# Kernel optimization log

Measured on AMD Instinct MI355X. Metric: run time of the kernel, lower is better.

Reference implementation:

```python
import jax, jax.numpy as jnp
import numpy as np

WH, WW = 12, 12
N_TOK = WH * WW          # 144
DIM = 512
HEADS = 16
NW = 64                  # windows per image
B_ = 256                 # num_windows * batch
CPB_HIDDEN = 512


def _rel_tables():
    # continuous relative coords table (SwinV2 cpb input), shape (1, 2Wh-1, 2Ww-1, 2)
    ch = np.arange(-(WH - 1), WH, dtype=np.float32)
    cw = np.arange(-(WW - 1), WW, dtype=np.float32)
    gh, gw = np.meshgrid(ch, cw, indexing='ij')
    table = np.stack([gh, gw], axis=-1)[None]
    table[..., 0] /= (WH - 1)
    table[..., 1] /= (WW - 1)
    table *= 8.0
    table = np.sign(table) * np.log2(np.abs(table) + 1.0) / np.log2(8.0)
    # relative position index, shape (N, N), values in [0, (2Wh-1)*(2Ww-1))
    coords = np.stack(np.meshgrid(np.arange(WH), np.arange(WW), indexing='ij'))
    cf = coords.reshape(2, -1)
    rel = (cf[:, :, None] - cf[:, None, :]).transpose(1, 2, 0).astype(np.int64)
    rel[..., 0] += WH - 1
    rel[..., 1] += WW - 1
    rel[..., 0] *= 2 * WW - 1
    idx = rel.sum(-1)
    return table.astype(np.float32), idx


def setup_inputs() -> dict:
    key = jax.random.key(0)
    ks = jax.random.split(key, 10)
    table, idx = _rel_tables()
    x = jax.random.normal(ks[0], (B_, N_TOK, DIM), dtype=jnp.float32)
    # 0 / -100 additive mask (shifted-window style), shape (nW, N, N)
    mask = jnp.where(jax.random.uniform(ks[1], (NW, N_TOK, N_TOK)) < 0.9, 0.0, -100.0).astype(jnp.float32)
    s = 0.02
    return {
        'x': x,
        'mask': mask,
        'qkv_w': s * jax.random.normal(ks[2], (3 * DIM, DIM), dtype=jnp.float32),
        'qkv_b': jnp.zeros((3 * DIM,), dtype=jnp.float32),
        'proj_w': s * jax.random.normal(ks[3], (DIM, DIM), dtype=jnp.float32),
        'proj_b': jnp.zeros((DIM,), dtype=jnp.float32),
        'cpb_w1': s * jax.random.normal(ks[4], (CPB_HIDDEN, 2), dtype=jnp.float32),
        'cpb_b1': jnp.zeros((CPB_HIDDEN,), dtype=jnp.float32),
        'cpb_w2': s * jax.random.normal(ks[5], (HEADS, CPB_HIDDEN), dtype=jnp.float32),
        'rel_table': jnp.asarray(table),
        'rel_index': jnp.asarray(idx, dtype=jnp.int32),
    }


def reference(x, mask, qkv_w, qkv_b, proj_w, proj_b, cpb_w1, cpb_b1, cpb_w2, rel_table, rel_index):
    Bw, N, C = x.shape
    H = cpb_w2.shape[0]
    hd = C // H
    scale = hd ** -0.5
    qkv = (x @ qkv_w.T + qkv_b).reshape(Bw, N, 3, H, hd).transpose(2, 0, 3, 1, 4)
    q, k, v = qkv[0], qkv[1], qkv[2]          # each (Bw, H, N, hd)
    attn = jnp.einsum('bhnd,bhmd->bhnm', q * scale, k)
    # continuous relative position bias: MLP on coord table then gather
    tbl = jax.nn.relu(rel_table @ cpb_w1.T + cpb_b1) @ cpb_w2.T   # (1, 2Wh-1, 2Ww-1, H)
    tbl = tbl.reshape(-1, H)
    bias = tbl[rel_index.reshape(-1)].reshape(N, N, H).transpose(2, 0, 1)  # (H, N, N)
    attn = attn + bias[None]
    nW = mask.shape[0]
    attn = attn.reshape(Bw // nW, nW, H, N, N) + mask[None, :, None]
    attn = jax.nn.softmax(attn.reshape(Bw, H, N, N), axis=-1)
    out = jnp.einsum('bhnm,bhmd->bhnd', attn, v).transpose(0, 2, 1, 3).reshape(Bw, N, C)
    return out @ proj_w.T + proj_b
```

## Files before the change

### kernel.cpp

```cpp
#include <hip/hip_runtime.h>


using f32x4  = __attribute__((ext_vector_type(4))) float;
using bf16x8 = __attribute__((ext_vector_type(8))) short;

__device__ __forceinline__ unsigned short f2bf(float f) {
  unsigned u = __float_as_uint(f);
  u = (u + 0x7fffu + ((u >> 16) & 1u)) >> 16;
  return (unsigned short)u;
}
__device__ __forceinline__ float bf2f(unsigned short s) {
  return __uint_as_float(((unsigned)s) << 16);
}

typedef __attribute__((address_space(1))) unsigned int as1_u32;
typedef __attribute__((address_space(3))) unsigned int as3_u32;

__device__ __forceinline__ void gll16(const void* g, void* l) {
  __builtin_amdgcn_global_load_lds((const as1_u32*)g, (as3_u32*)l, 16, 0, 0);
}

__global__ void cvt_f32_bf16(const float4* __restrict__ in,
                             unsigned short* __restrict__ out, int n4) {
  int i = blockIdx.x * blockDim.x + threadIdx.x;
  int stride = gridDim.x * blockDim.x;
  for (; i < n4; i += stride) {
    float4 v = in[i];
    ushort4 o;
    o.x = f2bf(v.x); o.y = f2bf(v.y); o.z = f2bf(v.z); o.w = f2bf(v.w);
    *(ushort4*)(out + (size_t)i * 4) = o;
  }
}

__global__ void cpb_mlp(const float* __restrict__ tbl_in,
                        const float* __restrict__ w1,
                        const float* __restrict__ b1,
                        const float* __restrict__ w2,
                        float* __restrict__ tbl_out) {
  __shared__ float hid[512];
  const int p = blockIdx.x;
  const int t = threadIdx.x;
  float t0 = tbl_in[p * 2 + 0], t1 = tbl_in[p * 2 + 1];
  float hv = fmaf(w1[t * 2 + 0], t0, fmaf(w1[t * 2 + 1], t1, b1[t]));
  hid[t] = fmaxf(hv, 0.f);
  __syncthreads();
  const int head = t >> 5, j = t & 31;
  float partial = 0.f;
  for (int i = j; i < 512; i += 32) partial += hid[i] * w2[head * 512 + i];
#pragma unroll
  for (int mk = 16; mk >= 1; mk >>= 1) partial += __shfl_xor(partial, mk, 32);
  if (j == 0) tbl_out[p * 16 + head] = partial;
}

__global__ void bias_gather(const float* __restrict__ tbl,
                            const int* __restrict__ idx,
                            unsigned short* __restrict__ bias_bf) {
  int f = blockIdx.x * 256 + threadIdx.x;
  if (f >= 16 * 20736) return;
  int h = f / 20736;
  int p = f - h * 20736;
  bias_bf[f] = f2bf(tbl[idx[p] * 16 + h]);
}

template <bool OUT_BF16, bool QSCALE>
__global__ __launch_bounds__(256) void gemm_bt_k(
    const unsigned short* __restrict__ A, const unsigned short* __restrict__ B,
    const float* __restrict__ bias, void* __restrict__ C, int N, int K) {
  __shared__ __align__(16) unsigned short As[128 * 32];
  __shared__ __align__(16) unsigned short Bs[128 * 32];
  const int tid = threadIdx.x;
  const int wave = tid >> 6, lane = tid & 63;
  const int m0 = blockIdx.y << 7, n0 = blockIdx.x << 7;
  const int wr = wave >> 1, wc = wave & 1;
  const int l15 = lane & 15, l4 = lane >> 4;

  f32x4 acc[4][4] = {};

  const unsigned short* gA = A + (size_t)(m0 + wave * 32 + (lane >> 2)) * K + (lane & 3) * 8;
  const unsigned short* gB = B + (size_t)(n0 + wave * 32 + (lane >> 2)) * K + (lane & 3) * 8;
  unsigned short* lA = As + wave * 32 * 32;
  unsigned short* lB = Bs + wave * 32 * 32;

  for (int k0 = 0; k0 < K; k0 += 32) {
    __syncthreads();
    gll16(gA + k0, lA);
    gll16(gA + k0 + (size_t)16 * K, lA + 16 * 32);
    gll16(gB + k0, lB);
    gll16(gB + k0 + (size_t)16 * K, lB + 16 * 32);
    __syncthreads();
    bf16x8 af[4], bfr[4];
#pragma unroll
    for (int t = 0; t < 4; ++t) {
      af[t]  = *(const bf16x8*)(As + (wr * 64 + t * 16 + l15) * 32 + l4 * 8);
      bfr[t] = *(const bf16x8*)(Bs + (wc * 64 + t * 16 + l15) * 32 + l4 * 8);
    }
#pragma unroll
    for (int i = 0; i < 4; ++i)
#pragma unroll
      for (int j = 0; j < 4; ++j)
        acc[i][j] = __builtin_amdgcn_mfma_f32_16x16x32_bf16(af[i], bfr[j], acc[i][j], 0, 0, 0);
  }

#pragma unroll
  for (int i = 0; i < 4; ++i) {
    int rowb = m0 + wr * 64 + i * 16 + l4 * 4;
#pragma unroll
    for (int j = 0; j < 4; ++j) {
      int col = n0 + wc * 64 + j * 16 + l15;
      float bv = bias[col];
#pragma unroll
      for (int r = 0; r < 4; ++r) {
        size_t off = (size_t)(rowb + r) * N + col;
        float v = acc[i][j][r] + bv;
        if (QSCALE && col < 512) v *= 0.17677669529663688f;
        if (OUT_BF16) ((unsigned short*)C)[off] = f2bf(v);
        else          ((float*)C)[off] = v;
      }
    }
  }
}

__global__ __launch_bounds__(256) void attn_k(
    const unsigned short* __restrict__ qkv,
    const unsigned short* __restrict__ maskbf,
    const unsigned short* __restrict__ biasbf,
    unsigned short* __restrict__ aout) {
  __shared__ __align__(16) unsigned short SP[144 * 152];
  __shared__ __align__(16) unsigned short Vt[32 * 152];

  const int h = blockIdx.x, b = blockIdx.y;
  const int tid = threadIdx.x;
  const int wave = tid >> 6, lane = tid & 63;
  const int l15 = lane & 15, l4 = lane >> 4;
  const size_t base = (size_t)b * 144 * 1536;

  for (int c = tid; c < 576; c += 256) {
    int n = c >> 2, p = c & 3;
    uint4 v = *(const uint4*)(qkv + base + (size_t)n * 1536 + 1024 + h * 32 + p * 8);
    unsigned short tmp[8];
    *(uint4*)tmp = v;
#pragma unroll
    for (int j = 0; j < 8; ++j) Vt[(p * 8 + j) * 152 + n] = tmp[j];
  }

  const unsigned short* mrow = maskbf + (size_t)(b & 63) * 20736;
  const unsigned short* brow = biasbf + (size_t)h * 20736;
  for (int tt = wave; tt < 81; tt += 4) {
    int ti = tt / 9, tj = tt - ti * 9;
    bf16x8 aq = *(const bf16x8*)(qkv + base + (size_t)(ti * 16 + l15) * 1536 + h * 32 + l4 * 8);
    bf16x8 bk = *(const bf16x8*)(qkv + base + (size_t)(tj * 16 + l15) * 1536 + 512 + h * 32 + l4 * 8);
    f32x4 c;
#pragma unroll
    for (int r = 0; r < 4; ++r) {
      int rr = ti * 16 + l4 * 4 + r, cc = tj * 16 + l15;
      c[r] = bf2f(mrow[rr * 144 + cc]) + bf2f(brow[rr * 144 + cc]);
    }
    c = __builtin_amdgcn_mfma_f32_16x16x32_bf16(aq, bk, c, 0, 0, 0);
#pragma unroll
    for (int r = 0; r < 4; ++r)
      SP[(ti * 16 + l4 * 4 + r) * 152 + tj * 16 + l15] = f2bf(c[r]);
  }
  __syncthreads();

  {
    const int g = tid >> 4, j = tid & 15;
#pragma unroll
    for (int rr = 0; rr < 9; ++rr) {
      int r = g + rr * 16;
      float lv[9];
      float mx = -3.0e38f;
#pragma unroll
      for (int c2 = 0; c2 < 9; ++c2) {
        lv[c2] = bf2f(SP[r * 152 + j + c2 * 16]);
        mx = fmaxf(mx, lv[c2]);
      }
#pragma unroll
      for (int mk = 8; mk >= 1; mk >>= 1) mx = fmaxf(mx, __shfl_xor(mx, mk, 16));
      float sum = 0.f;
#pragma unroll
      for (int c2 = 0; c2 < 9; ++c2) {
        lv[c2] = __expf(lv[c2] - mx);
        sum += lv[c2];
      }
#pragma unroll
      for (int mk = 8; mk >= 1; mk >>= 1) sum += __shfl_xor(sum, mk, 16);
      float inv = 1.f / sum;
#pragma unroll
      for (int c2 = 0; c2 < 9; ++c2)
        SP[r * 152 + j + c2 * 16] = f2bf(lv[c2] * inv);
    }
  }
  __syncthreads();

  for (int tt = wave; tt < 18; tt += 4) {
    int ti = tt >> 1, dj = tt & 1;
    f32x4 c = {0.f, 0.f, 0.f, 0.f};
    const unsigned short* pa = SP + (ti * 16 + l15) * 152;
    const unsigned short* vb = Vt + (dj * 16 + l15) * 152;
#pragma unroll
    for (int ks = 0; ks < 4; ++ks) {
      bf16x8 ap = *(const bf16x8*)(pa + ks * 32 + l4 * 8);
      bf16x8 bv = *(const bf16x8*)(vb + ks * 32 + l4 * 8);
      c = __builtin_amdgcn_mfma_f32_16x16x32_bf16(ap, bv, c, 0, 0, 0);
    }
    {
      bf16x8 ap = {}, bv = {};
      if (l4 < 2) {
        ap = *(const bf16x8*)(pa + 128 + l4 * 8);
        bv = *(const bf16x8*)(vb + 128 + l4 * 8);
      }
      c = __builtin_amdgcn_mfma_f32_16x16x32_bf16(ap, bv, c, 0, 0, 0);
    }
#pragma unroll
    for (int r = 0; r < 4; ++r) {
      int n = ti * 16 + l4 * 4 + r;
      int d = dj * 16 + l15;
      aout[((size_t)(b * 144 + n)) * 512 + h * 32 + d] = f2bf(c[r]);
    }
  }
}

extern "C" void kernel_launch(void* const* d_in, const int* in_sizes, int n_in,
                              void* d_out, int out_size, void* d_ws, size_t ws_size,
                              hipStream_t stream) {
  const float* x        = (const float*)d_in[0];
  const float* mask     = (const float*)d_in[1];
  const float* qkv_w    = (const float*)d_in[2];
  const float* qkv_b    = (const float*)d_in[3];
  const float* proj_w   = (const float*)d_in[4];
  const float* proj_b   = (const float*)d_in[5];
  const float* cpb_w1   = (const float*)d_in[6];
  const float* cpb_b1   = (const float*)d_in[7];
  const float* cpb_w2   = (const float*)d_in[8];
  const float* rel_tab  = (const float*)d_in[9];
  const int*   rel_idx  = (const int*)d_in[10];
  float* out = (float*)d_out;

  char* ws = (char*)d_ws;
  unsigned short* x_bf    = (unsigned short*)(ws);
  unsigned short* wq_bf   = (unsigned short*)(ws + 37748736);
  unsigned short* wp_bf   = (unsigned short*)(ws + 39321600);
  unsigned short* qkv_ws  = (unsigned short*)(ws + 39845888);
  unsigned short* attn_ws = (unsigned short*)(ws + 153092096);
  float*          tbl_ws  = (float*)(ws + 190840832);
  unsigned short* maskbf  = (unsigned short*)(ws + 190874688);
  unsigned short* biasbf  = (unsigned short*)(ws + 193528896);

  cvt_f32_bf16<<<2048, 256, 0, stream>>>((const float4*)x, x_bf, 4718592);
  cvt_f32_bf16<<<768, 256, 0, stream>>>((const float4*)qkv_w, wq_bf, 196608);
  cvt_f32_bf16<<<256, 256, 0, stream>>>((const float4*)proj_w, wp_bf, 65536);
  cvt_f32_bf16<<<1296, 256, 0, stream>>>((const float4*)mask, maskbf, 331776);

  cpb_mlp<<<529, 512, 0, stream>>>(rel_tab, cpb_w1, cpb_b1, cpb_w2, tbl_ws);
  bias_gather<<<1296, 256, 0, stream>>>(tbl_ws, rel_idx, biasbf);

  gemm_bt_k<true, true><<<dim3(12, 288), 256, 0, stream>>>(
      x_bf, wq_bf, qkv_b, (void*)qkv_ws, 1536, 512);

  attn_k<<<dim3(16, 256), 256, 0, stream>>>(qkv_ws, maskbf, biasbf, attn_ws);

  gemm_bt_k<false, false><<<dim3(4, 288), 256, 0, stream>>>(
      attn_ws, wp_bf, proj_b, (void*)out, 512, 512);
}
```

Baseline: 434.0 us.

## Fuse softmax into QK^T row-tile loop with transposed MFMA and register-resident scores

Each wave now computes a full 16x144 row strip of scores with swapped MFMA operands (K as A, Q as B), so every lane holds its row's scores in registers. Softmax runs there with only two cross-lane shuffles, and one bf16 write of the probabilities replaces the bf16 score round trip through shared memory plus one barrier. Mask and bias loads become vectorized ushort4 reads, and the V transpose load is reindexed for better coalescing. The cost is only 9 row tiles spread across 4 waves, so load is uneven (waves 0 gets 3 tiles), and register pressure rises from 36 accumulators per lane.

```diff
diff --git a/kernel.cpp b/kernel.cpp
--- a/kernel.cpp
+++ b/kernel.cpp
@@ -125,7 +125,7 @@
     const unsigned short* __restrict__ maskbf,
     const unsigned short* __restrict__ biasbf,
     unsigned short* __restrict__ aout) {
-  __shared__ __align__(16) unsigned short SP[144 * 152];
+  __shared__ __align__(16) unsigned short P[144 * 152];
   __shared__ __align__(16) unsigned short Vt[32 * 152];
 
   const int h = blockIdx.x, b = blockIdx.y;
@@ -135,67 +135,70 @@
   const size_t base = (size_t)b * 144 * 1536;
 
   for (int c = tid; c < 576; c += 256) {
-    int n = c >> 2, p = c & 3;
-    uint4 v = *(const uint4*)(qkv + base + (size_t)n * 1536 + 1024 + h * 32 + p * 8);
+    int dblk = c / 144;
+    int m = c - dblk * 144;
+    uint4 v = *(const uint4*)(qkv + base + (size_t)m * 1536 + 1024 + h * 32 + dblk * 8);
     unsigned short tmp[8];
     *(uint4*)tmp = v;
 #pragma unroll
-    for (int j = 0; j < 8; ++j) Vt[(p * 8 + j) * 152 + n] = tmp[j];
+    for (int j = 0; j < 8; ++j) Vt[(dblk * 8 + j) * 152 + m] = tmp[j];
   }
 
   const unsigned short* mrow = maskbf + (size_t)(b & 63) * 20736;
   const unsigned short* brow = biasbf + (size_t)h * 20736;
-  for (int tt = wave; tt < 81; tt += 4) {
-    int ti = tt / 9, tj = tt - ti * 9;
-    bf16x8 aq = *(const bf16x8*)(qkv + base + (size_t)(ti * 16 + l15) * 1536 + h * 32 + l4 * 8);
-    bf16x8 bk = *(const bf16x8*)(qkv + base + (size_t)(tj * 16 + l15) * 1536 + 512 + h * 32 + l4 * 8);
-    f32x4 c;
-#pragma unroll
-    for (int r = 0; r < 4; ++r) {
-      int rr = ti * 16 + l4 * 4 + r, cc = tj * 16 + l15;
-      c[r] = bf2f(mrow[rr * 144 + cc]) + bf2f(brow[rr * 144 + cc]);
-    }
-    c = __builtin_amdgcn_mfma_f32_16x16x32_bf16(aq, bk, c, 0, 0, 0);
-#pragma unroll
-    for (int r = 0; r < 4; ++r)
-      SP[(ti * 16 + l4 * 4 + r) * 152 + tj * 16 + l15] = f2bf(c[r]);
+  for (int rt = wave; rt < 9; rt += 4) {
+    const int n = rt * 16 + l15;
+    bf16x8 qf = *(const bf16x8*)(qkv + base + (size_t)n * 1536 + h * 32 + l4 * 8);
+    f32x4 acc[9];
+#pragma unroll
+    for (int kt = 0; kt < 9; ++kt) {
+      bf16x8 kf = *(const bf16x8*)(qkv + base + (size_t)(kt * 16 + l15) * 1536 + 512 + h * 32 + l4 * 8);
+      const int mq = kt * 16 + l4 * 4;
+      ushort4 mv = *(const ushort4*)(mrow + n * 144 + mq);
+      ushort4 bv = *(const ushort4*)(brow + n * 144 + mq);
+      f32x4 ci;
+      ci[0] = bf2f(mv.x) + bf2f(bv.x);
+      ci[1] = bf2f(mv.y) + bf2f(bv.y);
+      ci[2] = bf2f(mv.z) + bf2f(bv.z);
+      ci[3] = bf2f(mv.w) + bf2f(bv.w);
+      acc[kt] = __builtin_amdgcn_mfma_f32_16x16x32_bf16(kf, qf, ci, 0, 0, 0);
+    }
+    float mx = -3.0e38f;
+#pragma unroll
+    for (int kt = 0; kt < 9; ++kt)
+#pragma unroll
+      for (int r = 0; r < 4; ++r) mx = fmaxf(mx, acc[kt][r]);
+    mx = fmaxf(mx, __shfl_xor(mx, 16));
+    mx = fmaxf(mx, __shfl_xor(mx, 32));
+    float sum = 0.f;
+#pragma unroll
+    for (int kt = 0; kt < 9; ++kt)
+#pragma unroll
+      for (int r = 0; r < 4; ++r) {
+        float p = __expf(acc[kt][r] - mx);
+        acc[kt][r] = p;
+        sum += p;
+      }
+    sum += __shfl_xor(sum, 16);
+    sum += __shfl_xor(sum, 32);
+    float inv = 1.0f / sum;
+    unsigned short* prow = P + n * 152;
+#pragma unroll
+    for (int kt = 0; kt < 9; ++kt) {
+      ushort4 o;
+      o.x = f2bf(acc[kt][0] * inv);
+      o.y = f2bf(acc[kt][1] * inv);
+      o.z = f2bf(acc[kt][2] * inv);
+      o.w = f2bf(acc[kt][3] * inv);
+      *(ushort4*)(prow + kt * 16 + l4 * 4) = o;
+    }
   }
   __syncthreads();
 
-  {
-    const int g = tid >> 4, j = tid & 15;
-#pragma unroll
-    for (int rr = 0; rr < 9; ++rr) {
-      int r = g + rr * 16;
-      float lv[9];
-      float mx = -3.0e38f;
-#pragma unroll
-      for (int c2 = 0; c2 < 9; ++c2) {
-        lv[c2] = bf2f(SP[r * 152 + j + c2 * 16]);
-        mx = fmaxf(mx, lv[c2]);
-      }
-#pragma unroll
-      for (int mk = 8; mk >= 1; mk >>= 1) mx = fmaxf(mx, __shfl_xor(mx, mk, 16));
-      float sum = 0.f;
-#pragma unroll
-      for (int c2 = 0; c2 < 9; ++c2) {
-        lv[c2] = __expf(lv[c2] - mx);
-        sum += lv[c2];
-      }
-#pragma unroll
-      for (int mk = 8; mk >= 1; mk >>= 1) sum += __shfl_xor(sum, mk, 16);
-      float inv = 1.f / sum;
-#pragma unroll
-      for (int c2 = 0; c2 < 9; ++c2)
-        SP[r * 152 + j + c2 * 16] = f2bf(lv[c2] * inv);
-    }
-  }
-  __syncthreads();
-
   for (int tt = wave; tt < 18; tt += 4) {
-    int ti = tt >> 1, dj = tt & 1;
+    int rt = tt >> 1, dj = tt & 1;
     f32x4 c = {0.f, 0.f, 0.f, 0.f};
-    const unsigned short* pa = SP + (ti * 16 + l15) * 152;
+    const unsigned short* pa = P + (rt * 16 + l15) * 152;
     const unsigned short* vb = Vt + (dj * 16 + l15) * 152;
 #pragma unroll
     for (int ks = 0; ks < 4; ++ks) {
@@ -213,7 +216,7 @@
     }
 #pragma unroll
     for (int r = 0; r < 4; ++r) {
-      int n = ti * 16 + l4 * 4 + r;
+      int n = rt * 16 + l4 * 4 + r;
       int d = dj * 16 + l15;
       aout[((size_t)(b * 144 + n)) * 512 + h * 32 + d] = f2bf(c[r]);
     }
```

Result: faster. 407.6 us (-6.1%).
